# Performance work log

Hardware: AMD Instinct MI355X
Metric: run time of the kernel (lower is better)

Reference implementation:

```python
import jax, jax.numpy as jnp
import numpy as np

PH = 12        # planning_horizon
B = 16         # batch
H = 256        # belief dim
Z = 64         # state dim
CAND = 512     # candidates
TOPK = 64      # top_candidates
ITERS = 3      # optimisation_iters
NTOOLS = 36    # num_tools
CONT = 2       # cont_action_size (hard-coded in source)
MIN_A, MAX_A = -1.0, 1.0


def setup_inputs() -> dict:
    ks = jax.random.split(jax.random.key(0), 9)
    s = 0.05  # weight scale keeps tanh in its linear-ish regime
    return {
        "belief": jax.random.normal(ks[0], (B, H), jnp.float32),
        "state": jax.random.normal(ks[1], (B, Z), jnp.float32),
        "Wb": jax.random.normal(ks[2], (H, H), jnp.float32) * s,
        "Wa": jax.random.normal(ks[3], (3, H), jnp.float32) * s,
        "bb": jnp.zeros((H,), jnp.float32),
        "Ws": jax.random.normal(ks[4], (H, Z), jnp.float32) * s,
        "bs": jnp.zeros((Z,), jnp.float32),
        "wrb": jax.random.normal(ks[5], (H,), jnp.float32) * s,
        "wrs": jax.random.normal(ks[6], (Z,), jnp.float32) * s,
    }


def reference(belief, state, Wb, Wa, bb, Ws, bs, wrb, wrs):
    # expand to (B*CAND, .) exactly like unsqueeze+expand+reshape (row-repeat)
    b0 = jnp.repeat(belief, CAND, axis=0)  # (B*CAND, H)
    s0 = jnp.repeat(state, CAND, axis=0)   # (B*CAND, Z)

    action_mean = jnp.zeros((PH, B, 1, CONT), jnp.float32)
    action_std = jnp.ones((PH, B, 1, CONT), jnp.float32)
    freq = jnp.ones((PH, B, 1, NTOOLS), jnp.float32)

    key = jax.random.key(42)
    for it in range(ITERS):
        k_disc, k_noise, key = jax.random.split(key, 3)
        # multinomial(freq, CAND, replacement=True) per (PH*B) row
        logits = jnp.log(freq.reshape(-1, NTOOLS))            # (PH*B, NTOOLS)
        disc = jax.random.categorical(k_disc, logits, shape=(CAND, PH * B)).T
        disc = disc.reshape(PH, B * CAND, 1).astype(jnp.float32)
        # continuous: mean + std * N(0,1), clamped
        noise = jax.random.normal(k_noise, (PH, B, CAND, CONT), jnp.float32)
        cont = jnp.clip(action_mean + action_std * noise, MIN_A, MAX_A)
        cont = cont.reshape(PH, B * CAND, CONT)
        actions = jnp.concatenate([disc, cont], axis=-1)       # (PH, B*CAND, 3)

        # rollout: stand-in recurrent transition + linear reward
        def step(carry, a_t):
            b, s_ = carry
            b = jnp.tanh(b @ Wb + a_t @ Wa + bb)
            s_ = jnp.tanh(b @ Ws + bs)
            return (b, s_), (b, s_)

        _, (beliefs, states) = jax.lax.scan(step, (b0, s0), actions)
        returns = (beliefs @ wrb + states @ wrs).sum(axis=0)   # (B*CAND,)

        # top-k candidates per batch element
        _, idx = jax.lax.top_k(returns.reshape(B, CAND), TOPK)  # (B, TOPK)
        actions_r = actions.reshape(PH, B, CAND, 1 + CONT)
        best = jnp.take_along_axis(actions_r, idx[None, :, :, None], axis=2)  # (PH,B,TOPK,3)

        cont_best = best[..., 1:]
        action_mean = cont_best.mean(axis=2, keepdims=True)
        action_std = jnp.std(cont_best, axis=2, keepdims=True)  # unbiased=False

        # batched histogram over TOPK discrete actions (histc with unit bins),
        # +1 smoothing, normalize -- one fused pass instead of PH*B histc calls
        dints = best[..., 0].astype(jnp.int32)                  # (PH, B, TOPK)
        hist = jax.nn.one_hot(dints, NTOOLS, dtype=jnp.float32).sum(axis=2) + 1.0
        freq = (hist / hist.sum(axis=-1, keepdims=True))[:, :, None, :]

    disc_final = jnp.argmax(freq[0, :, 0, :], axis=-1).astype(jnp.float32)[:, None]  # (B,1)
    cont_final = action_mean[0, :, 0, :]                                             # (B,CONT)
    return jnp.concatenate([disc_final, cont_final], axis=1)                         # (B,3)
```

## Files before the change

kernel.cpp:

```cpp
#include <hip/hip_runtime.h>
#include <cstdint>
#include <cmath>

#define PARTITIONABLE 1

constexpr int kPH = 12;
constexpr int kB = 16;
constexpr int kH = 256;
constexpr int kZ = 64;
constexpr int kCand = 512;
constexpr int kTopK = 64;
constexpr int kTools = 36;
constexpr int kRT = kB * kCand;
constexpr uint32_t kDiscTotal = (uint32_t)kCand * kPH * kB * kTools;
constexpr uint32_t kContTotal = (uint32_t)kPH * kB * kCand * 2;

constexpr int kRowsB = 16;
constexpr int kStrideB = 20;

__host__ __device__ inline void tf2x32(uint32_t k0, uint32_t k1,
                                       uint32_t x0, uint32_t x1,
                                       uint32_t& o0, uint32_t& o1) {
  uint32_t ks2 = k0 ^ k1 ^ 0x1BD11BDAu;
  x0 += k0; x1 += k1;
#define TFROT(v, d) (((v) << (d)) | ((v) >> (32 - (d))))
#define TFR(r) { x0 += x1; x1 = TFROT(x1, r); x1 ^= x0; }
  TFR(13) TFR(15) TFR(26) TFR(6)
  x0 += k1;  x1 += ks2 + 1u;
  TFR(17) TFR(29) TFR(16) TFR(24)
  x0 += ks2; x1 += k0 + 2u;
  TFR(13) TFR(15) TFR(26) TFR(6)
  x0 += k0;  x1 += k1 + 3u;
  TFR(17) TFR(29) TFR(16) TFR(24)
  x0 += k1;  x1 += ks2 + 4u;
  TFR(13) TFR(15) TFR(26) TFR(6)
  x0 += ks2; x1 += k0 + 5u;
#undef TFR
#undef TFROT
  o0 = x0; o1 = x1;
}

__device__ inline uint32_t jax_bits32(uint32_t k0, uint32_t k1,
                                      uint32_t idx, uint32_t total) {
#if PARTITIONABLE
  (void)total;
  uint32_t y0, y1;
  tf2x32(k0, k1, 0u, idx, y0, y1);
  return y0 ^ y1;
#else
  uint32_t half = total >> 1;
  uint32_t y0, y1;
  if (idx < half) { tf2x32(k0, k1, idx, idx + half, y0, y1); return y0; }
  else            { tf2x32(k0, k1, idx - half, idx, y0, y1); return y1; }
#endif
}

static void host_split3(uint32_t k0, uint32_t k1, uint32_t out[3][2]) {
#if PARTITIONABLE
  for (uint32_t i = 0; i < 3; ++i)
    tf2x32(k0, k1, 0u, i, out[i][0], out[i][1]);
#else
  uint32_t a0,a1,b0,b1,c0,c1;
  tf2x32(k0, k1, 0u, 3u, a0, a1);
  tf2x32(k0, k1, 1u, 4u, b0, b1);
  tf2x32(k0, k1, 2u, 5u, c0, c1);
  out[0][0]=a0; out[0][1]=b0;
  out[1][0]=c0; out[1][1]=a1;
  out[2][0]=b1; out[2][1]=c1;
#endif
}

__device__ inline float erfinv_xla(float x) {
  float xx = x * x;
  float w = -(float)log1p((double)(-xx));
  float p;
  if (w < 5.0f) {
    float ww = w - 2.5f;
    p = 2.81022636e-08f;
    p = fmaf(p, ww, 3.43273939e-07f);
    p = fmaf(p, ww, -3.5233877e-06f);
    p = fmaf(p, ww, -4.39150654e-06f);
    p = fmaf(p, ww, 0.00021858087f);
    p = fmaf(p, ww, -0.00125372503f);
    p = fmaf(p, ww, -0.00417768164f);
    p = fmaf(p, ww, 0.246640727f);
    p = fmaf(p, ww, 1.50140941f);
  } else {
    float ww = sqrtf(w) - 3.0f;
    p = -0.000200214257f;
    p = fmaf(p, ww, 0.000100950558f);
    p = fmaf(p, ww, 0.00134934322f);
    p = fmaf(p, ww, -0.00367342844f);
    p = fmaf(p, ww, 0.00573950773f);
    p = fmaf(p, ww, -0.0076224613f);
    p = fmaf(p, ww, 0.00943887047f);
    p = fmaf(p, ww, 1.00167406f);
    p = fmaf(p, ww, 2.83297682f);
  }
  return p * x;
}

__global__ __launch_bounds__(256) void k_sample_disc(
    uint32_t kd0, uint32_t kd1, const float* __restrict__ lfreq,
    float* __restrict__ discA, int it0) {
  int gid = blockIdx.x * 256 + threadIdx.x;
  if (gid >= kCand * kPH * kB) return;
  int c = gid / (kPH * kB);
  int j = gid - c * (kPH * kB);
  int best = 0;
  if (it0) {
    uint32_t bm = 0u;
    for (int t = 0; t < kTools; ++t) {
      uint32_t bits = jax_bits32(kd0, kd1, (uint32_t)(gid * kTools + t), kDiscTotal);
      uint32_t m = bits >> 9;
      if (t == 0 || m > bm) { bm = m; best = t; }
    }
  } else {
    const float* lf = lfreq + j * kTools;
    float bv = 0.0f;
    for (int t = 0; t < kTools; ++t) {
      uint32_t bits = jax_bits32(kd0, kd1, (uint32_t)(gid * kTools + t), kDiscTotal);
      float u = __uint_as_float((bits >> 9) | 0x3F800000u) - 1.0f;
      if (u == 0.0f) u = 1.17549435e-38f;
      float l1 = (float)log((double)u);
      float g = -(float)log((double)(-l1));
      float val = g + lf[t];
      if (t == 0 || val > bv) { bv = val; best = t; }
    }
  }
  int ph = j >> 4, b = j & 15;
  discA[ph * kRT + b * kCand + c] = (float)best;
}

__global__ __launch_bounds__(256) void k_sample_cont(
    uint32_t kn0, uint32_t kn1, const float* __restrict__ meanv,
    const float* __restrict__ stdv, float* __restrict__ contA, int it0) {
  int gid = blockIdx.x * 256 + threadIdx.x;
  if (gid >= (int)kContTotal) return;
  uint32_t bits = jax_bits32(kn0, kn1, (uint32_t)gid, kContTotal);
  float f = __uint_as_float((bits >> 9) | 0x3F800000u) - 1.0f;
  const float lo = -0.99999994f;
  float u = fmaxf(lo, f * 2.0f + lo);
  float n = __uint_as_float(0x3FB504F3u) * erfinv_xla(u);
  int d = gid & 1;
  int c = (gid >> 1) & (kCand - 1);
  int rest = gid >> 10;
  int ph = rest >> 4, b = rest & 15;
  float m, s;
  if (it0) { m = 0.0f; s = 1.0f; }
  else {
    m = meanv[rest * 2 + d];
    s = stdv[rest * 2 + d];
  }
  float x = m + s * n;
  x = fminf(fmaxf(x, -1.0f), 1.0f);
  contA[(ph * kRT + b * kCand + c) * 2 + d] = x;
}

__global__ __launch_bounds__(512, 4) void k_rollout(
    const float* __restrict__ belief,
    const float* __restrict__ discA, const float* __restrict__ contA,
    const float* __restrict__ Wb, const float* __restrict__ Wa,
    const float* __restrict__ bbv_, const float* __restrict__ Ws,
    const float* __restrict__ bs_, const float* __restrict__ wrb,
    const float* __restrict__ wrs, float* __restrict__ ret) {
  __shared__ float sBc[kH * kStrideB];
  __shared__ float pT[kRowsB * kH];
  __shared__ float sPT[kRowsB * kZ];
  __shared__ float sAD[kPH][kRowsB];
  __shared__ float sA0[kPH][kRowsB];
  __shared__ float sA1[kPH][kRowsB];
  __shared__ float sret[kRowsB];

  const int tid = threadIdx.x;
  const int row0 = blockIdx.x * kRowsB;
  const int batch = row0 >> 9;

  const int w = tid >> 6;
  const int kw = w >> 2;
  const int wc = w & 3;
  const int lane = tid & 63;
  const int lr = lane >> 4;
  const int lc = lane & 15;
  const int r0 = lr * 4;
  const int c0 = wc * 64 + lc * 4;
  const int zc = wc * 16 + lc;
  const int kbase = kw * 128;

  const float4 bb4  = *reinterpret_cast<const float4*>(&bbv_[c0]);
  const float4 wa04 = *reinterpret_cast<const float4*>(&Wa[c0]);
  const float4 wa14 = *reinterpret_cast<const float4*>(&Wa[kH + c0]);
  const float4 wa24 = *reinterpret_cast<const float4*>(&Wa[2 * kH + c0]);
  const float4 wrb4 = *reinterpret_cast<const float4*>(&wrb[c0]);
  const float bsv = bs_[zc], wrsv = wrs[zc];

  if (tid < kH) {
    float v = belief[batch * kH + tid];
    #pragma unroll
    for (int r = 0; r < kRowsB; ++r) sBc[tid * kStrideB + r] = v;
  }
  for (int i = tid; i < kPH * kRowsB; i += 512) {
    int ph = i >> 4, r = i & 15;
    int gr = row0 + r;
    sAD[ph][r] = discA[ph * kRT + gr];
    sA0[ph][r] = contA[(ph * kRT + gr) * 2 + 0];
    sA1[ph][r] = contA[(ph * kRT + gr) * 2 + 1];
  }
  if (tid < kRowsB) sret[tid] = 0.0f;

  float rsum[4] = {0.0f, 0.0f, 0.0f, 0.0f};
  float ssum[4] = {0.0f, 0.0f, 0.0f, 0.0f};
  __syncthreads();

  const float* bK = sBc + kbase * kStrideB + r0;
  const float* wB = Wb + (size_t)kbase * kH + c0;
  const float* wS = Ws + (size_t)kbase * kZ + zc;

  #pragma unroll 1
  for (int ph = 0; ph < kPH; ++ph) {
    float acc[4][4];
    #pragma unroll
    for (int r = 0; r < 4; ++r)
      #pragma unroll
      for (int c = 0; c < 4; ++c) acc[r][c] = 0.0f;
    #pragma unroll 4
    for (int k = 0; k < 128; ++k) {
      float4 bv = *reinterpret_cast<const float4*>(bK + k * kStrideB);
      float4 wv = *reinterpret_cast<const float4*>(wB + k * kH);
      acc[0][0] = fmaf(bv.x, wv.x, acc[0][0]);
      acc[0][1] = fmaf(bv.x, wv.y, acc[0][1]);
      acc[0][2] = fmaf(bv.x, wv.z, acc[0][2]);
      acc[0][3] = fmaf(bv.x, wv.w, acc[0][3]);
      acc[1][0] = fmaf(bv.y, wv.x, acc[1][0]);
      acc[1][1] = fmaf(bv.y, wv.y, acc[1][1]);
      acc[1][2] = fmaf(bv.y, wv.z, acc[1][2]);
      acc[1][3] = fmaf(bv.y, wv.w, acc[1][3]);
      acc[2][0] = fmaf(bv.z, wv.x, acc[2][0]);
      acc[2][1] = fmaf(bv.z, wv.y, acc[2][1]);
      acc[2][2] = fmaf(bv.z, wv.z, acc[2][2]);
      acc[2][3] = fmaf(bv.z, wv.w, acc[2][3]);
      acc[3][0] = fmaf(bv.w, wv.x, acc[3][0]);
      acc[3][1] = fmaf(bv.w, wv.y, acc[3][1]);
      acc[3][2] = fmaf(bv.w, wv.z, acc[3][2]);
      acc[3][3] = fmaf(bv.w, wv.w, acc[3][3]);
    }
    if (kw == 1) {
      #pragma unroll
      for (int r = 0; r < 4; ++r)
        *reinterpret_cast<float4*>(&pT[(r0 + r) * kH + c0]) =
            make_float4(acc[r][0], acc[r][1], acc[r][2], acc[r][3]);
    }
    __syncthreads();
    if (kw == 0) {
      #pragma unroll
      for (int r = 0; r < 4; ++r) {
        float4 p = *reinterpret_cast<const float4*>(&pT[(r0 + r) * kH + c0]);
        float aD = sAD[ph][r0 + r], a0 = sA0[ph][r0 + r], a1 = sA1[ph][r0 + r];
        float t0 = acc[r][0] + p.x + bb4.x + aD * wa04.x + a0 * wa14.x + a1 * wa24.x;
        float t1 = acc[r][1] + p.y + bb4.y + aD * wa04.y + a0 * wa14.y + a1 * wa24.y;
        float t2 = acc[r][2] + p.z + bb4.z + aD * wa04.z + a0 * wa14.z + a1 * wa24.z;
        float t3 = acc[r][3] + p.w + bb4.w + aD * wa04.w + a0 * wa14.w + a1 * wa24.w;
        acc[r][0] = tanhf(t0);
        acc[r][1] = tanhf(t1);
        acc[r][2] = tanhf(t2);
        acc[r][3] = tanhf(t3);
      }
      #pragma unroll
      for (int c = 0; c < 4; ++c)
        *reinterpret_cast<float4*>(&sBc[(c0 + c) * kStrideB + r0]) =
            make_float4(acc[0][c], acc[1][c], acc[2][c], acc[3][c]);
      #pragma unroll
      for (int r = 0; r < 4; ++r) {
        rsum[r] = fmaf(acc[r][0], wrb4.x, rsum[r]);
        rsum[r] = fmaf(acc[r][1], wrb4.y, rsum[r]);
        rsum[r] = fmaf(acc[r][2], wrb4.z, rsum[r]);
        rsum[r] = fmaf(acc[r][3], wrb4.w, rsum[r]);
      }
    }
    __syncthreads();

    float sa[4] = {0.0f, 0.0f, 0.0f, 0.0f};
    #pragma unroll 8
    for (int k = 0; k < 128; ++k) {
      float4 bv = *reinterpret_cast<const float4*>(bK + k * kStrideB);
      float wv = wS[k * kZ];
      sa[0] = fmaf(bv.x, wv, sa[0]);
      sa[1] = fmaf(bv.y, wv, sa[1]);
      sa[2] = fmaf(bv.z, wv, sa[2]);
      sa[3] = fmaf(bv.w, wv, sa[3]);
    }
    if (kw == 1) {
      #pragma unroll
      for (int r = 0; r < 4; ++r) sPT[(r0 + r) * kZ + zc] = sa[r];
    }
    __syncthreads();
    if (kw == 0) {
      #pragma unroll
      for (int r = 0; r < 4; ++r) {
        float sv = tanhf(sa[r] + sPT[(r0 + r) * kZ + zc] + bsv);
        ssum[r] = fmaf(sv, wrsv, ssum[r]);
      }
    }
  }

  if (kw == 0) {
    #pragma unroll
    for (int r = 0; r < 4; ++r) {
      float v = rsum[r] + ssum[r];
      v += __shfl_xor(v, 1, 64);
      v += __shfl_xor(v, 2, 64);
      v += __shfl_xor(v, 4, 64);
      v += __shfl_xor(v, 8, 64);
      if (lc == 0) atomicAdd(&sret[r0 + r], v);
    }
  }
  __syncthreads();
  if (tid < kRowsB) ret[row0 + tid] = sret[tid];
}

__global__ __launch_bounds__(256) void k_topk_stats(
    const float* __restrict__ ret, const float* __restrict__ discA,
    const float* __restrict__ contA, float* __restrict__ freq,
    float* __restrict__ lfreq, float* __restrict__ meanv,
    float* __restrict__ stdv) {
  __shared__ float rv[kCand];
  __shared__ int selc[kTopK];
  __shared__ int hist[kTools];
  const int b = blockIdx.x, tid = threadIdx.x;
  for (int i = tid; i < kCand; i += 256) rv[i] = ret[b * kCand + i];
  __syncthreads();
  for (int c = tid; c < kCand; c += 256) {
    float v = rv[c];
    int rank = 0;
    for (int o = 0; o < kCand; ++o) {
      float vo = rv[o];
      rank += ((vo > v) || (vo == v && o < c)) ? 1 : 0;
    }
    if (rank < kTopK) selc[rank] = c;
  }
  __syncthreads();
  for (int ph = 0; ph < kPH; ++ph) {
    if (tid < kTools) hist[tid] = 0;
    __syncthreads();
    if (tid < kTopK) {
      int c = selc[tid];
      int idx = ph * kRT + b * kCand + c;
      int d = (int)discA[idx];
      atomicAdd(&hist[d], 1);
      float c0 = contA[idx * 2 + 0];
      float c1 = contA[idx * 2 + 1];
      float s0 = c0, s1 = c1;
      #pragma unroll
      for (int sh = 1; sh < 64; sh <<= 1) {
        s0 += __shfl_xor(s0, sh, 64);
        s1 += __shfl_xor(s1, sh, 64);
      }
      float m0 = s0 * (1.0f / 64.0f);
      float m1 = s1 * (1.0f / 64.0f);
      float d0 = c0 - m0, d1 = c1 - m1;
      float q0 = d0 * d0, q1 = d1 * d1;
      #pragma unroll
      for (int sh = 1; sh < 64; sh <<= 1) {
        q0 += __shfl_xor(q0, sh, 64);
        q1 += __shfl_xor(q1, sh, 64);
      }
      if (tid == 0) {
        int o = (ph * kB + b) * 2;
        meanv[o + 0] = m0;
        meanv[o + 1] = m1;
        stdv[o + 0] = sqrtf(q0 * (1.0f / 64.0f));
        stdv[o + 1] = sqrtf(q1 * (1.0f / 64.0f));
      }
    }
    __syncthreads();
    if (tid < kTools) {
      float fq = (float)(hist[tid] + 1) / 100.0f;
      int o = (ph * kB + b) * kTools + tid;
      freq[o] = fq;
      lfreq[o] = (float)log((double)fq);
    }
    __syncthreads();
  }
}

__global__ void k_final(const float* __restrict__ freq,
                        const float* __restrict__ meanv,
                        float* __restrict__ out) {
  int b = threadIdx.x;
  if (b < kB) {
    const float* f = freq + b * kTools;
    int best = 0; float bv = f[0];
    for (int t = 1; t < kTools; ++t)
      if (f[t] > bv) { bv = f[t]; best = t; }
    out[b * 3 + 0] = (float)best;
    out[b * 3 + 1] = meanv[b * 2 + 0];
    out[b * 3 + 2] = meanv[b * 2 + 1];
  }
}

extern "C" void kernel_launch(void* const* d_in, const int* in_sizes, int n_in,
                              void* d_out, int out_size, void* d_ws, size_t ws_size,
                              hipStream_t stream) {
  (void)in_sizes; (void)n_in; (void)out_size; (void)ws_size;
  const float* belief = (const float*)d_in[0];
  const float* Wb  = (const float*)d_in[2];
  const float* Wa  = (const float*)d_in[3];
  const float* bb  = (const float*)d_in[4];
  const float* Ws  = (const float*)d_in[5];
  const float* bs  = (const float*)d_in[6];
  const float* wrb = (const float*)d_in[7];
  const float* wrs = (const float*)d_in[8];
  float* out = (float*)d_out;

  float* w = (float*)d_ws;
  float* discA = w;
  float* contA = discA + kPH * kRT;
  float* ret   = contA + kPH * kRT * 2;
  float* freq  = ret + kRT;
  float* lfreq = freq + kPH * kB * kTools;
  float* meanv = lfreq + kPH * kB * kTools;
  float* stdv  = meanv + kPH * kB * 2;

  uint32_t key0 = 0u, key1 = 42u;
  for (int it = 0; it < 3; ++it) {
    uint32_t ks[3][2];
    host_split3(key0, key1, ks);
    int it0 = (it == 0) ? 1 : 0;
    k_sample_disc<<<dim3((kCand * kPH * kB + 255) / 256), dim3(256), 0, stream>>>(
        ks[0][0], ks[0][1], lfreq, discA, it0);
    k_sample_cont<<<dim3((kContTotal + 255) / 256), dim3(256), 0, stream>>>(
        ks[1][0], ks[1][1], meanv, stdv, contA, it0);
    k_rollout<<<dim3(kRT / kRowsB), dim3(512), 0, stream>>>(
        belief, discA, contA, Wb, Wa, bb, Ws, bs, wrb, wrs, ret);
    k_topk_stats<<<dim3(kB), dim3(256), 0, stream>>>(
        ret, discA, contA, freq, lfreq, meanv, stdv);
    key0 = ks[2][0]; key1 = ks[2][1];
  }
  k_final<<<dim3(1), dim3(64), 0, stream>>>(freq, meanv, out);
}
```

Baseline: 1.083 ms.

## Drop split-K in rollout, use 128-thread blocks with 4x8 register tiles

The rollout kernel drops its two-way K split, which needed shared-memory partial-sum buffers and extra barriers per step. Each thread now covers the full K=256 reduction over a 4x8 output tile, and the block shrinks to 128 threads. This removes the cross-warp reduction and the pT/sPT traffic and reuses each loaded weight value across more rows. In exchange each thread runs twice as many serial FMAs, register pressure rises, and there are fewer threads per block to hide latency.

```diff
diff --git a/kernel.cpp b/kernel.cpp
--- a/kernel.cpp
+++ b/kernel.cpp
@@ -157,7 +157,7 @@
   contA[(ph * kRT + b * kCand + c) * 2 + d] = x;
 }
 
-__global__ __launch_bounds__(512, 4) void k_rollout(
+__global__ __launch_bounds__(128) void k_rollout(
     const float* __restrict__ belief,
     const float* __restrict__ discA, const float* __restrict__ contA,
     const float* __restrict__ Wb, const float* __restrict__ Wa,
@@ -165,8 +165,6 @@
     const float* __restrict__ bs_, const float* __restrict__ wrb,
     const float* __restrict__ wrs, float* __restrict__ ret) {
   __shared__ float sBc[kH * kStrideB];
-  __shared__ float pT[kRowsB * kH];
-  __shared__ float sPT[kRowsB * kZ];
   __shared__ float sAD[kPH][kRowsB];
   __shared__ float sA0[kPH][kRowsB];
   __shared__ float sA1[kPH][kRowsB];
@@ -176,30 +174,33 @@
   const int row0 = blockIdx.x * kRowsB;
   const int batch = row0 >> 9;
 
-  const int w = tid >> 6;
-  const int kw = w >> 2;
-  const int wc = w & 3;
+  const int wave = tid >> 6;
   const int lane = tid & 63;
-  const int lr = lane >> 4;
-  const int lc = lane & 15;
-  const int r0 = lr * 4;
-  const int c0 = wc * 64 + lc * 4;
-  const int zc = wc * 16 + lc;
-  const int kbase = kw * 128;
-
-  const float4 bb4  = *reinterpret_cast<const float4*>(&bbv_[c0]);
-  const float4 wa04 = *reinterpret_cast<const float4*>(&Wa[c0]);
-  const float4 wa14 = *reinterpret_cast<const float4*>(&Wa[kH + c0]);
-  const float4 wa24 = *reinterpret_cast<const float4*>(&Wa[2 * kH + c0]);
-  const float4 wrb4 = *reinterpret_cast<const float4*>(&wrb[c0]);
-  const float bsv = bs_[zc], wrsv = wrs[zc];
-
-  if (tid < kH) {
-    float v = belief[batch * kH + tid];
+  const int rg = lane & 3;
+  const int cg = lane >> 2;
+  const int r0 = rg * 4;
+  const int c0 = wave * 128 + cg * 8;
+  const int zc = wave * 32 + cg * 2;
+
+  const float4 bbA  = *reinterpret_cast<const float4*>(&bbv_[c0]);
+  const float4 bbB  = *reinterpret_cast<const float4*>(&bbv_[c0 + 4]);
+  const float4 wa0A = *reinterpret_cast<const float4*>(&Wa[c0]);
+  const float4 wa0B = *reinterpret_cast<const float4*>(&Wa[c0 + 4]);
+  const float4 wa1A = *reinterpret_cast<const float4*>(&Wa[kH + c0]);
+  const float4 wa1B = *reinterpret_cast<const float4*>(&Wa[kH + c0 + 4]);
+  const float4 wa2A = *reinterpret_cast<const float4*>(&Wa[2 * kH + c0]);
+  const float4 wa2B = *reinterpret_cast<const float4*>(&Wa[2 * kH + c0 + 4]);
+  const float4 wrbA = *reinterpret_cast<const float4*>(&wrb[c0]);
+  const float4 wrbB = *reinterpret_cast<const float4*>(&wrb[c0 + 4]);
+  const float2 bs2  = *reinterpret_cast<const float2*>(&bs_[zc]);
+  const float2 wrs2 = *reinterpret_cast<const float2*>(&wrs[zc]);
+
+  for (int c = tid; c < kH; c += 128) {
+    float v = belief[batch * kH + c];
     #pragma unroll
-    for (int r = 0; r < kRowsB; ++r) sBc[tid * kStrideB + r] = v;
-  }
-  for (int i = tid; i < kPH * kRowsB; i += 512) {
+    for (int r = 0; r < kRowsB; ++r) sBc[c * kStrideB + r] = v;
+  }
+  for (int i = tid; i < kPH * kRowsB; i += 128) {
     int ph = i >> 4, r = i & 15;
     int gr = row0 + r;
     sAD[ph][r] = discA[ph * kRT + gr];
@@ -209,110 +210,95 @@
   if (tid < kRowsB) sret[tid] = 0.0f;
 
   float rsum[4] = {0.0f, 0.0f, 0.0f, 0.0f};
-  float ssum[4] = {0.0f, 0.0f, 0.0f, 0.0f};
   __syncthreads();
 
-  const float* bK = sBc + kbase * kStrideB + r0;
-  const float* wB = Wb + (size_t)kbase * kH + c0;
-  const float* wS = Ws + (size_t)kbase * kZ + zc;
+  const float* bK = sBc + r0;
+  const float* wB = Wb + c0;
+  const float* wS = Ws + zc;
 
   #pragma unroll 1
   for (int ph = 0; ph < kPH; ++ph) {
-    float acc[4][4];
+    float acc[4][8];
     #pragma unroll
     for (int r = 0; r < 4; ++r)
       #pragma unroll
-      for (int c = 0; c < 4; ++c) acc[r][c] = 0.0f;
+      for (int c = 0; c < 8; ++c) acc[r][c] = 0.0f;
+
     #pragma unroll 4
-    for (int k = 0; k < 128; ++k) {
+    for (int k = 0; k < kH; ++k) {
       float4 bv = *reinterpret_cast<const float4*>(bK + k * kStrideB);
-      float4 wv = *reinterpret_cast<const float4*>(wB + k * kH);
-      acc[0][0] = fmaf(bv.x, wv.x, acc[0][0]);
-      acc[0][1] = fmaf(bv.x, wv.y, acc[0][1]);
-      acc[0][2] = fmaf(bv.x, wv.z, acc[0][2]);
-      acc[0][3] = fmaf(bv.x, wv.w, acc[0][3]);
-      acc[1][0] = fmaf(bv.y, wv.x, acc[1][0]);
-      acc[1][1] = fmaf(bv.y, wv.y, acc[1][1]);
-      acc[1][2] = fmaf(bv.y, wv.z, acc[1][2]);
-      acc[1][3] = fmaf(bv.y, wv.w, acc[1][3]);
-      acc[2][0] = fmaf(bv.z, wv.x, acc[2][0]);
-      acc[2][1] = fmaf(bv.z, wv.y, acc[2][1]);
-      acc[2][2] = fmaf(bv.z, wv.z, acc[2][2]);
-      acc[2][3] = fmaf(bv.z, wv.w, acc[2][3]);
-      acc[3][0] = fmaf(bv.w, wv.x, acc[3][0]);
-      acc[3][1] = fmaf(bv.w, wv.y, acc[3][1]);
-      acc[3][2] = fmaf(bv.w, wv.z, acc[3][2]);
-      acc[3][3] = fmaf(bv.w, wv.w, acc[3][3]);
-    }
-    if (kw == 1) {
+      float4 w0 = *reinterpret_cast<const float4*>(wB + (size_t)k * kH);
+      float4 w1 = *reinterpret_cast<const float4*>(wB + (size_t)k * kH + 4);
+      float bvr[4] = {bv.x, bv.y, bv.z, bv.w};
+      float wvc[8] = {w0.x, w0.y, w0.z, w0.w, w1.x, w1.y, w1.z, w1.w};
       #pragma unroll
       for (int r = 0; r < 4; ++r)
-        *reinterpret_cast<float4*>(&pT[(r0 + r) * kH + c0]) =
-            make_float4(acc[r][0], acc[r][1], acc[r][2], acc[r][3]);
+        #pragma unroll
+        for (int c = 0; c < 8; ++c)
+          acc[r][c] = fmaf(bvr[r], wvc[c], acc[r][c]);
+    }
+
+    float bn[4][8];
+    {
+      float bbv[8]  = {bbA.x, bbA.y, bbA.z, bbA.w, bbB.x, bbB.y, bbB.z, bbB.w};
+      float wa0v[8] = {wa0A.x, wa0A.y, wa0A.z, wa0A.w, wa0B.x, wa0B.y, wa0B.z, wa0B.w};
+      float wa1v[8] = {wa1A.x, wa1A.y, wa1A.z, wa1A.w, wa1B.x, wa1B.y, wa1B.z, wa1B.w};
+      float wa2v[8] = {wa2A.x, wa2A.y, wa2A.z, wa2A.w, wa2B.x, wa2B.y, wa2B.z, wa2B.w};
+      #pragma unroll
+      for (int r = 0; r < 4; ++r) {
+        float aD = sAD[ph][r0 + r];
+        float a0 = sA0[ph][r0 + r];
+        float a1 = sA1[ph][r0 + r];
+        #pragma unroll
+        for (int c = 0; c < 8; ++c) {
+          float t = acc[r][c] + bbv[c] + aD * wa0v[c] + a0 * wa1v[c] + a1 * wa2v[c];
+          bn[r][c] = tanhf(t);
+        }
+      }
+      float wrbv[8] = {wrbA.x, wrbA.y, wrbA.z, wrbA.w, wrbB.x, wrbB.y, wrbB.z, wrbB.w};
+      #pragma unroll
+      for (int r = 0; r < 4; ++r)
+        #pragma unroll
+        for (int c = 0; c < 8; ++c)
+          rsum[r] = fmaf(bn[r][c], wrbv[c], rsum[r]);
     }
     __syncthreads();
-    if (kw == 0) {
+
+    #pragma unroll
+    for (int c = 0; c < 8; ++c)
+      *reinterpret_cast<float4*>(&sBc[(c0 + c) * kStrideB + r0]) =
+          make_float4(bn[0][c], bn[1][c], bn[2][c], bn[3][c]);
+    __syncthreads();
+
+    float sa[4][2] = {{0.0f,0.0f},{0.0f,0.0f},{0.0f,0.0f},{0.0f,0.0f}};
+    #pragma unroll 4
+    for (int k = 0; k < kH; ++k) {
+      float4 bv = *reinterpret_cast<const float4*>(bK + k * kStrideB);
+      float2 wv = *reinterpret_cast<const float2*>(wS + (size_t)k * kZ);
+      float bvr[4] = {bv.x, bv.y, bv.z, bv.w};
       #pragma unroll
       for (int r = 0; r < 4; ++r) {
-        float4 p = *reinterpret_cast<const float4*>(&pT[(r0 + r) * kH + c0]);
-        float aD = sAD[ph][r0 + r], a0 = sA0[ph][r0 + r], a1 = sA1[ph][r0 + r];
-        float t0 = acc[r][0] + p.x + bb4.x + aD * wa04.x + a0 * wa14.x + a1 * wa24.x;
-        float t1 = acc[r][1] + p.y + bb4.y + aD * wa04.y + a0 * wa14.y + a1 * wa24.y;
-        float t2 = acc[r][2] + p.z + bb4.z + aD * wa04.z + a0 * wa14.z + a1 * wa24.z;
-        float t3 = acc[r][3] + p.w + bb4.w + aD * wa04.w + a0 * wa14.w + a1 * wa24.w;
-        acc[r][0] = tanhf(t0);
-        acc[r][1] = tanhf(t1);
-        acc[r][2] = tanhf(t2);
-        acc[r][3] = tanhf(t3);
+        sa[r][0] = fmaf(bvr[r], wv.x, sa[r][0]);
+        sa[r][1] = fmaf(bvr[r], wv.y, sa[r][1]);
       }
-      #pragma unroll
-      for (int c = 0; c < 4; ++c)
-        *reinterpret_cast<float4*>(&sBc[(c0 + c) * kStrideB + r0]) =
-            make_float4(acc[0][c], acc[1][c], acc[2][c], acc[3][c]);
-      #pragma unroll
-      for (int r = 0; r < 4; ++r) {
-        rsum[r] = fmaf(acc[r][0], wrb4.x, rsum[r]);
-        rsum[r] = fmaf(acc[r][1], wrb4.y, rsum[r]);
-        rsum[r] = fmaf(acc[r][2], wrb4.z, rsum[r]);
-        rsum[r] = fmaf(acc[r][3], wrb4.w, rsum[r]);
-      }
-    }
-    __syncthreads();
-
-    float sa[4] = {0.0f, 0.0f, 0.0f, 0.0f};
-    #pragma unroll 8
-    for (int k = 0; k < 128; ++k) {
-      float4 bv = *reinterpret_cast<const float4*>(bK + k * kStrideB);
-      float wv = wS[k * kZ];
-      sa[0] = fmaf(bv.x, wv, sa[0]);
-      sa[1] = fmaf(bv.y, wv, sa[1]);
-      sa[2] = fmaf(bv.z, wv, sa[2]);
-      sa[3] = fmaf(bv.w, wv, sa[3]);
-    }
-    if (kw == 1) {
-      #pragma unroll
-      for (int r = 0; r < 4; ++r) sPT[(r0 + r) * kZ + zc] = sa[r];
-    }
-    __syncthreads();
-    if (kw == 0) {
-      #pragma unroll
-      for (int r = 0; r < 4; ++r) {
-        float sv = tanhf(sa[r] + sPT[(r0 + r) * kZ + zc] + bsv);
-        ssum[r] = fmaf(sv, wrsv, ssum[r]);
-      }
-    }
-  }
-
-  if (kw == 0) {
+    }
     #pragma unroll
     for (int r = 0; r < 4; ++r) {
-      float v = rsum[r] + ssum[r];
-      v += __shfl_xor(v, 1, 64);
-      v += __shfl_xor(v, 2, 64);
-      v += __shfl_xor(v, 4, 64);
-      v += __shfl_xor(v, 8, 64);
-      if (lc == 0) atomicAdd(&sret[r0 + r], v);
-    }
+      float s0 = tanhf(sa[r][0] + bs2.x);
+      float s1 = tanhf(sa[r][1] + bs2.y);
+      rsum[r] = fmaf(s0, wrs2.x, rsum[r]);
+      rsum[r] = fmaf(s1, wrs2.y, rsum[r]);
+    }
+  }
+
+  #pragma unroll
+  for (int r = 0; r < 4; ++r) {
+    float v = rsum[r];
+    v += __shfl_xor(v, 4, 64);
+    v += __shfl_xor(v, 8, 64);
+    v += __shfl_xor(v, 16, 64);
+    v += __shfl_xor(v, 32, 64);
+    if (cg == 0) atomicAdd(&sret[r0 + r], v);
   }
   __syncthreads();
   if (tid < kRowsB) ret[row0 + tid] = sret[tid];
@@ -430,7 +416,7 @@
         ks[0][0], ks[0][1], lfreq, discA, it0);
     k_sample_cont<<<dim3((kContTotal + 255) / 256), dim3(256), 0, stream>>>(
         ks[1][0], ks[1][1], meanv, stdv, contA, it0);
-    k_rollout<<<dim3(kRT / kRowsB), dim3(512), 0, stream>>>(
+    k_rollout<<<dim3(kRT / kRowsB), dim3(128), 0, stream>>>(
         belief, discA, contA, Wb, Wa, bb, Ws, bs, wrb, wrs, ret);
     k_topk_stats<<<dim3(kB), dim3(256), 0, stream>>>(
         ret, discA, contA, freq, lfreq, meanv, stdv);
```

Result: slower. 2.219 ms (+105.0%).

## Remap rollout GEMV threads to 8x4 tiles with four-way K split

Applied to the files above, without the earlier changes.

The rollout kernel's thread mapping is restructured. Each wave now covers all 256 hidden columns (state columns in the state phase) for 8 rows, and the K dimension is split four ways instead of two. Belief reads from shared memory become wave-uniform broadcasts, Wb loads are fully coalesced, and the padded stride is dropped. The per-row return is reduced with a full-wave shuffle instead of shared-memory atomics. In exchange there are three partial-sum buffers to combine, and the tanh epilogue runs on only two waves.

```diff
diff --git a/kernel.cpp b/kernel.cpp
--- a/kernel.cpp
+++ b/kernel.cpp
@@ -16,7 +16,6 @@
 constexpr uint32_t kContTotal = (uint32_t)kPH * kB * kCand * 2;
 
 constexpr int kRowsB = 16;
-constexpr int kStrideB = 20;
 
 __host__ __device__ inline void tf2x32(uint32_t k0, uint32_t k1,
                                        uint32_t x0, uint32_t x1,
@@ -164,40 +163,42 @@
     const float* __restrict__ bbv_, const float* __restrict__ Ws,
     const float* __restrict__ bs_, const float* __restrict__ wrb,
     const float* __restrict__ wrs, float* __restrict__ ret) {
-  __shared__ float sBc[kH * kStrideB];
-  __shared__ float pT[kRowsB * kH];
-  __shared__ float sPT[kRowsB * kZ];
+  __shared__ float sBc[kH * kRowsB];
+  __shared__ float pT[3][kRowsB][kH];
+  __shared__ float sPT[3][kRowsB][kZ];
   __shared__ float sAD[kPH][kRowsB];
   __shared__ float sA0[kPH][kRowsB];
   __shared__ float sA1[kPH][kRowsB];
-  __shared__ float sret[kRowsB];
 
   const int tid = threadIdx.x;
   const int row0 = blockIdx.x * kRowsB;
   const int batch = row0 >> 9;
 
   const int w = tid >> 6;
-  const int kw = w >> 2;
-  const int wc = w & 3;
   const int lane = tid & 63;
-  const int lr = lane >> 4;
-  const int lc = lane & 15;
-  const int r0 = lr * 4;
-  const int c0 = wc * 64 + lc * 4;
-  const int zc = wc * 16 + lc;
-  const int kbase = kw * 128;
+  const int rowg = w & 1;
+  const int ks = w >> 1;
+  const int r0 = rowg * 8;
+  const int c0 = lane * 4;
+
+  const int sks = tid >> 7;
+  const int zg = lane;
 
   const float4 bb4  = *reinterpret_cast<const float4*>(&bbv_[c0]);
   const float4 wa04 = *reinterpret_cast<const float4*>(&Wa[c0]);
   const float4 wa14 = *reinterpret_cast<const float4*>(&Wa[kH + c0]);
   const float4 wa24 = *reinterpret_cast<const float4*>(&Wa[2 * kH + c0]);
   const float4 wrb4 = *reinterpret_cast<const float4*>(&wrb[c0]);
-  const float bsv = bs_[zc], wrsv = wrs[zc];
+  const float bsv = bs_[zg], wrsv = wrs[zg];
 
   if (tid < kH) {
     float v = belief[batch * kH + tid];
-    #pragma unroll
-    for (int r = 0; r < kRowsB; ++r) sBc[tid * kStrideB + r] = v;
+    float4 v4 = make_float4(v, v, v, v);
+    float* p = &sBc[tid * kRowsB];
+    *reinterpret_cast<float4*>(p + 0) = v4;
+    *reinterpret_cast<float4*>(p + 4) = v4;
+    *reinterpret_cast<float4*>(p + 8) = v4;
+    *reinterpret_cast<float4*>(p + 12) = v4;
   }
   for (int i = tid; i < kPH * kRowsB; i += 512) {
     int ph = i >> 4, r = i & 15;
@@ -206,116 +207,125 @@
     sA0[ph][r] = contA[(ph * kRT + gr) * 2 + 0];
     sA1[ph][r] = contA[(ph * kRT + gr) * 2 + 1];
   }
-  if (tid < kRowsB) sret[tid] = 0.0f;
-
-  float rsum[4] = {0.0f, 0.0f, 0.0f, 0.0f};
-  float ssum[4] = {0.0f, 0.0f, 0.0f, 0.0f};
+
+  float rsum[8] = {0,0,0,0,0,0,0,0};
+  float ssum[8] = {0,0,0,0,0,0,0,0};
   __syncthreads();
 
-  const float* bK = sBc + kbase * kStrideB + r0;
-  const float* wB = Wb + (size_t)kbase * kH + c0;
-  const float* wS = Ws + (size_t)kbase * kZ + zc;
+  const float* bKb = sBc + (ks * 64) * kRowsB + r0;
+  const float* wB  = Wb + (size_t)(ks * 64) * kH + c0;
+  const float* bKs = sBc + (sks * 64) * kRowsB + r0;
+  const float* wS  = Ws + (size_t)(sks * 64) * kZ + zg;
 
   #pragma unroll 1
   for (int ph = 0; ph < kPH; ++ph) {
-    float acc[4][4];
+    float acc[8][4];
     #pragma unroll
-    for (int r = 0; r < 4; ++r)
-      #pragma unroll
-      for (int c = 0; c < 4; ++c) acc[r][c] = 0.0f;
+    for (int i = 0; i < 8; ++i)
+      #pragma unroll
+      for (int j = 0; j < 4; ++j) acc[i][j] = 0.0f;
+
     #pragma unroll 4
-    for (int k = 0; k < 128; ++k) {
-      float4 bv = *reinterpret_cast<const float4*>(bK + k * kStrideB);
-      float4 wv = *reinterpret_cast<const float4*>(wB + k * kH);
-      acc[0][0] = fmaf(bv.x, wv.x, acc[0][0]);
-      acc[0][1] = fmaf(bv.x, wv.y, acc[0][1]);
-      acc[0][2] = fmaf(bv.x, wv.z, acc[0][2]);
-      acc[0][3] = fmaf(bv.x, wv.w, acc[0][3]);
-      acc[1][0] = fmaf(bv.y, wv.x, acc[1][0]);
-      acc[1][1] = fmaf(bv.y, wv.y, acc[1][1]);
-      acc[1][2] = fmaf(bv.y, wv.z, acc[1][2]);
-      acc[1][3] = fmaf(bv.y, wv.w, acc[1][3]);
-      acc[2][0] = fmaf(bv.z, wv.x, acc[2][0]);
-      acc[2][1] = fmaf(bv.z, wv.y, acc[2][1]);
-      acc[2][2] = fmaf(bv.z, wv.z, acc[2][2]);
-      acc[2][3] = fmaf(bv.z, wv.w, acc[2][3]);
-      acc[3][0] = fmaf(bv.w, wv.x, acc[3][0]);
-      acc[3][1] = fmaf(bv.w, wv.y, acc[3][1]);
-      acc[3][2] = fmaf(bv.w, wv.z, acc[3][2]);
-      acc[3][3] = fmaf(bv.w, wv.w, acc[3][3]);
-    }
-    if (kw == 1) {
-      #pragma unroll
-      for (int r = 0; r < 4; ++r)
-        *reinterpret_cast<float4*>(&pT[(r0 + r) * kH + c0]) =
-            make_float4(acc[r][0], acc[r][1], acc[r][2], acc[r][3]);
-    }
-    __syncthreads();
-    if (kw == 0) {
-      #pragma unroll
-      for (int r = 0; r < 4; ++r) {
-        float4 p = *reinterpret_cast<const float4*>(&pT[(r0 + r) * kH + c0]);
-        float aD = sAD[ph][r0 + r], a0 = sA0[ph][r0 + r], a1 = sA1[ph][r0 + r];
-        float t0 = acc[r][0] + p.x + bb4.x + aD * wa04.x + a0 * wa14.x + a1 * wa24.x;
-        float t1 = acc[r][1] + p.y + bb4.y + aD * wa04.y + a0 * wa14.y + a1 * wa24.y;
-        float t2 = acc[r][2] + p.z + bb4.z + aD * wa04.z + a0 * wa14.z + a1 * wa24.z;
-        float t3 = acc[r][3] + p.w + bb4.w + aD * wa04.w + a0 * wa14.w + a1 * wa24.w;
-        acc[r][0] = tanhf(t0);
-        acc[r][1] = tanhf(t1);
-        acc[r][2] = tanhf(t2);
-        acc[r][3] = tanhf(t3);
-      }
-      #pragma unroll
-      for (int c = 0; c < 4; ++c)
-        *reinterpret_cast<float4*>(&sBc[(c0 + c) * kStrideB + r0]) =
-            make_float4(acc[0][c], acc[1][c], acc[2][c], acc[3][c]);
-      #pragma unroll
-      for (int r = 0; r < 4; ++r) {
-        rsum[r] = fmaf(acc[r][0], wrb4.x, rsum[r]);
-        rsum[r] = fmaf(acc[r][1], wrb4.y, rsum[r]);
-        rsum[r] = fmaf(acc[r][2], wrb4.z, rsum[r]);
-        rsum[r] = fmaf(acc[r][3], wrb4.w, rsum[r]);
-      }
-    }
-    __syncthreads();
-
-    float sa[4] = {0.0f, 0.0f, 0.0f, 0.0f};
-    #pragma unroll 8
-    for (int k = 0; k < 128; ++k) {
-      float4 bv = *reinterpret_cast<const float4*>(bK + k * kStrideB);
-      float wv = wS[k * kZ];
-      sa[0] = fmaf(bv.x, wv, sa[0]);
-      sa[1] = fmaf(bv.y, wv, sa[1]);
-      sa[2] = fmaf(bv.z, wv, sa[2]);
-      sa[3] = fmaf(bv.w, wv, sa[3]);
-    }
-    if (kw == 1) {
-      #pragma unroll
-      for (int r = 0; r < 4; ++r) sPT[(r0 + r) * kZ + zc] = sa[r];
-    }
-    __syncthreads();
-    if (kw == 0) {
-      #pragma unroll
-      for (int r = 0; r < 4; ++r) {
-        float sv = tanhf(sa[r] + sPT[(r0 + r) * kZ + zc] + bsv);
-        ssum[r] = fmaf(sv, wrsv, ssum[r]);
-      }
-    }
-  }
-
-  if (kw == 0) {
+    for (int k = 0; k < 64; ++k) {
+      float4 b0 = *reinterpret_cast<const float4*>(bKb + k * kRowsB);
+      float4 b1 = *reinterpret_cast<const float4*>(bKb + k * kRowsB + 4);
+      float4 wv = *reinterpret_cast<const float4*>(wB + (size_t)k * kH);
+      float bvr[8] = {b0.x, b0.y, b0.z, b0.w, b1.x, b1.y, b1.z, b1.w};
+      #pragma unroll
+      for (int i = 0; i < 8; ++i) {
+        acc[i][0] = fmaf(bvr[i], wv.x, acc[i][0]);
+        acc[i][1] = fmaf(bvr[i], wv.y, acc[i][1]);
+        acc[i][2] = fmaf(bvr[i], wv.z, acc[i][2]);
+        acc[i][3] = fmaf(bvr[i], wv.w, acc[i][3]);
+      }
+    }
+    if (ks != 0) {
+      #pragma unroll
+      for (int i = 0; i < 8; ++i)
+        *reinterpret_cast<float4*>(&pT[ks - 1][r0 + i][c0]) =
+            make_float4(acc[i][0], acc[i][1], acc[i][2], acc[i][3]);
+    }
+    __syncthreads();
+
+    if (ks == 0) {
+      #pragma unroll
+      for (int i = 0; i < 8; ++i) {
+        int r = r0 + i;
+        float4 p0 = *reinterpret_cast<const float4*>(&pT[0][r][c0]);
+        float4 p1 = *reinterpret_cast<const float4*>(&pT[1][r][c0]);
+        float4 p2 = *reinterpret_cast<const float4*>(&pT[2][r][c0]);
+        float aD = sAD[ph][r], a0 = sA0[ph][r], a1 = sA1[ph][r];
+        float t0 = ((acc[i][0] + p0.x) + p1.x) + p2.x + bb4.x
+                   + aD * wa04.x + a0 * wa14.x + a1 * wa24.x;
+        float t1 = ((acc[i][1] + p0.y) + p1.y) + p2.y + bb4.y
+                   + aD * wa04.y + a0 * wa14.y + a1 * wa24.y;
+        float t2 = ((acc[i][2] + p0.z) + p1.z) + p2.z + bb4.z
+                   + aD * wa04.z + a0 * wa14.z + a1 * wa24.z;
+        float t3 = ((acc[i][3] + p0.w) + p1.w) + p2.w + bb4.w
+                   + aD * wa04.w + a0 * wa14.w + a1 * wa24.w;
+        float n0 = tanhf(t0), n1 = tanhf(t1), n2 = tanhf(t2), n3 = tanhf(t3);
+        acc[i][0] = n0; acc[i][1] = n1; acc[i][2] = n2; acc[i][3] = n3;
+        rsum[i] = fmaf(n0, wrb4.x, rsum[i]);
+        rsum[i] = fmaf(n1, wrb4.y, rsum[i]);
+        rsum[i] = fmaf(n2, wrb4.z, rsum[i]);
+        rsum[i] = fmaf(n3, wrb4.w, rsum[i]);
+      }
+      #pragma unroll
+      for (int j = 0; j < 4; ++j) {
+        float* p = &sBc[(c0 + j) * kRowsB + r0];
+        *reinterpret_cast<float4*>(p) =
+            make_float4(acc[0][j], acc[1][j], acc[2][j], acc[3][j]);
+        *reinterpret_cast<float4*>(p + 4) =
+            make_float4(acc[4][j], acc[5][j], acc[6][j], acc[7][j]);
+      }
+    }
+    __syncthreads();
+
+    float sa[8] = {0,0,0,0,0,0,0,0};
+    #pragma unroll 4
+    for (int k = 0; k < 64; ++k) {
+      float4 b0 = *reinterpret_cast<const float4*>(bKs + k * kRowsB);
+      float4 b1 = *reinterpret_cast<const float4*>(bKs + k * kRowsB + 4);
+      float wv = wS[(size_t)k * kZ];
+      sa[0] = fmaf(b0.x, wv, sa[0]);
+      sa[1] = fmaf(b0.y, wv, sa[1]);
+      sa[2] = fmaf(b0.z, wv, sa[2]);
+      sa[3] = fmaf(b0.w, wv, sa[3]);
+      sa[4] = fmaf(b1.x, wv, sa[4]);
+      sa[5] = fmaf(b1.y, wv, sa[5]);
+      sa[6] = fmaf(b1.z, wv, sa[6]);
+      sa[7] = fmaf(b1.w, wv, sa[7]);
+    }
+    if (sks != 0) {
+      #pragma unroll
+      for (int i = 0; i < 8; ++i) sPT[sks - 1][r0 + i][zg] = sa[i];
+    }
+    __syncthreads();
+
+    if (sks == 0) {
+      #pragma unroll
+      for (int i = 0; i < 8; ++i) {
+        int r = r0 + i;
+        float t = ((sa[i] + sPT[0][r][zg]) + sPT[1][r][zg]) + sPT[2][r][zg] + bsv;
+        float sv = tanhf(t);
+        ssum[i] = fmaf(sv, wrsv, ssum[i]);
+      }
+    }
+  }
+
+  if (tid < 128) {
     #pragma unroll
-    for (int r = 0; r < 4; ++r) {
-      float v = rsum[r] + ssum[r];
+    for (int i = 0; i < 8; ++i) {
+      float v = rsum[i] + ssum[i];
       v += __shfl_xor(v, 1, 64);
       v += __shfl_xor(v, 2, 64);
       v += __shfl_xor(v, 4, 64);
       v += __shfl_xor(v, 8, 64);
-      if (lc == 0) atomicAdd(&sret[r0 + r], v);
-    }
-  }
-  __syncthreads();
-  if (tid < kRowsB) ret[row0 + tid] = sret[tid];
+      v += __shfl_xor(v, 16, 64);
+      v += __shfl_xor(v, 32, 64);
+      if (lane == 0) ret[row0 + r0 + i] = v;
+    }
+  }
 }
 
 __global__ __launch_bounds__(256) void k_topk_stats(
```

New measurement: 1.122 ms. +3.7%, slower.
